# Optimization experiments

Hardware: AMD Instinct MI355X
Metric: run time of the kernel (lower is better)

Reference implementation:

```python
import jax, jax.numpy as jnp
import numpy as np

IN, H1, H2 = 1600, 64, 32

def setup_inputs() -> dict:
    key = jax.random.key(0)
    ks = jax.random.split(key, 8)
    x = jax.random.normal(ks[0], (512, IN), dtype=jnp.float32)
    y = jax.random.normal(ks[1], (512, IN), dtype=jnp.float32)
    # Kaiming-ish init for the MLP params
    W1 = jax.random.normal(ks[2], (IN, H1), dtype=jnp.float32) / np.sqrt(IN)
    b1 = jnp.zeros((H1,), dtype=jnp.float32)
    W2 = jax.random.normal(ks[3], (H1, H2), dtype=jnp.float32) / np.sqrt(H1)
    b2 = jnp.zeros((H2,), dtype=jnp.float32)
    W3 = jax.random.normal(ks[4], (H2, 1), dtype=jnp.float32) / np.sqrt(H2)
    b3 = jnp.zeros((1,), dtype=jnp.float32)
    return {"x": x, "y": y, "W1": W1, "b1": b1, "W2": W2, "b2": b2, "W3": W3, "b3": b3}

def reference(x, y, W1, b1, W2, b2, W3, b3):
    # pairwise difference: (w, qw, 1600)
    d = x[:, None, :] - y[None, :, :]
    h = jax.nn.relu(jnp.einsum('wqi,ih->wqh', d, W1) + b1)   # (w,qw,64)
    h = jax.nn.relu(jnp.einsum('wqh,hk->wqk', h, W2) + b2)   # (w,qw,32)
    o = jax.nn.relu(jnp.einsum('wqk,ko->wqo', h, W3) + b3)   # (w,qw,1)
    return o[..., 0]                                          # (w,qw)
```

## Files before the change

kernel.cpp:

```cpp
#include <hip/hip_runtime.h>
#include <hip/hip_bf16.h>


#define IN_DIM 1600
#define H1D 64
#define H2D 32
#define NROW 512

typedef short bf16x8 __attribute__((ext_vector_type(8)));
typedef float f32x4 __attribute__((ext_vector_type(4)));

static __device__ __forceinline__ short f2bf(float v) {
  __hip_bfloat16 h = __float2bfloat16(v);
  return *reinterpret_cast<short*>(&h);
}

__global__ __launch_bounds__(1024) void proj_kernel(
    const float* __restrict__ x, const float* __restrict__ y,
    const float* __restrict__ W1, const float* __restrict__ b1,
    const float* __restrict__ W2,
    float* __restrict__ P, unsigned short* __restrict__ W2frag) {
  __shared__ float pacc[16 * 4 * 64];
  const int tid = threadIdx.x;
  const int lane = tid & 63;
  const int w = __builtin_amdgcn_readfirstlane(tid >> 6);
  const int row0 = (int)blockIdx.x * 4;
  const float* __restrict__ base = (row0 < NROW) ? x : y;
  const int r0 = (row0 < NROW) ? row0 : row0 - NROW;
  const int k0 = w * (IN_DIM / 16);

  const float* __restrict__ xr0 = base + (size_t)(r0 + 0) * IN_DIM + k0;
  const float* __restrict__ xr1 = base + (size_t)(r0 + 1) * IN_DIM + k0;
  const float* __restrict__ xr2 = base + (size_t)(r0 + 2) * IN_DIM + k0;
  const float* __restrict__ xr3 = base + (size_t)(r0 + 3) * IN_DIM + k0;
  const float* __restrict__ wp = W1 + (size_t)k0 * H1D + lane;

  float a0 = 0.f, a1 = 0.f, a2 = 0.f, a3 = 0.f;
#pragma unroll 4
  for (int i = 0; i < IN_DIM / 16; ++i) {
    const float wv = wp[i * H1D];
    a0 = fmaf(xr0[i], wv, a0);
    a1 = fmaf(xr1[i], wv, a1);
    a2 = fmaf(xr2[i], wv, a2);
    a3 = fmaf(xr3[i], wv, a3);
  }
  pacc[(w * 4 + 0) * 64 + lane] = a0;
  pacc[(w * 4 + 1) * 64 + lane] = a1;
  pacc[(w * 4 + 2) * 64 + lane] = a2;
  pacc[(w * 4 + 3) * 64 + lane] = a3;
  __syncthreads();

  if (tid < 256) {
    const int r = tid >> 6, h = tid & 63;
    float s = 0.f;
#pragma unroll
    for (int ww = 0; ww < 16; ++ww) s += pacc[(ww * 4 + r) * 64 + h];
    if (row0 < NROW) s += b1[h];
    P[(size_t)(row0 + r) * H1D + h] = s;
  } else if (blockIdx.x == 0 && tid >= 512) {
    const int t = tid - 512;
#pragma unroll
    for (int e = t; e < 4 * 64 * 8; e += 512) {
      const int f = e >> 9, l = (e >> 3) & 63, j = e & 7;
      const int ks = f & 1, nt = f >> 1;
      const int k = ks * 32 + (l >> 4) * 8 + j;
      const int n = nt * 16 + (l & 15);
      W2frag[e] = (unsigned short)f2bf(W2[k * H2D + n]);
    }
  }
}

__global__ __launch_bounds__(256) void pair_kernel(
    const float* __restrict__ P, const unsigned short* __restrict__ W2frag,
    const float* __restrict__ b2, const float* __restrict__ W3,
    const float* __restrict__ b3, float* __restrict__ out) {
  __shared__ float sX[16][68];
  __shared__ float sY[16][68];
  __shared__ float sO[16][16];

  const int tid = threadIdx.x;
  const int wave = tid >> 6, lane = tid & 63;
  const int l15 = lane & 15, l4 = lane >> 4;
  const int wb = blockIdx.x * 16, qb = blockIdx.y * 16;

  {
    const int r = tid >> 4, c = (tid & 15) * 4;
    const float4 vx = *reinterpret_cast<const float4*>(&P[(size_t)(wb + r) * H1D + c]);
    const float4 vy = *reinterpret_cast<const float4*>(&P[(size_t)(NROW + qb + r) * H1D + c]);
    *reinterpret_cast<float4*>(&sX[r][c]) = vx;
    *reinterpret_cast<float4*>(&sY[r][c]) = vy;
  }

  bf16x8 bfr[2][2];
#pragma unroll
  for (int nt = 0; nt < 2; ++nt)
#pragma unroll
    for (int ks = 0; ks < 2; ++ks)
      bfr[nt][ks] = *reinterpret_cast<const bf16x8*>(&W2frag[((nt * 2 + ks) * 64 + lane) * 8]);

  f32x4 acc[4][2];
  const float b2v0 = b2[l15], b2v1 = b2[16 + l15];
#pragma unroll
  for (int mt = 0; mt < 4; ++mt)
#pragma unroll
    for (int r = 0; r < 4; ++r) { acc[mt][0][r] = b2v0; acc[mt][1][r] = b2v1; }

  __syncthreads();

#pragma unroll
  for (int ks = 0; ks < 2; ++ks) {
    const int kb = ks * 32 + l4 * 8;
    const float4 y0 = *reinterpret_cast<const float4*>(&sY[l15][kb]);
    const float4 y1 = *reinterpret_cast<const float4*>(&sY[l15][kb + 4]);
#pragma unroll
    for (int mt = 0; mt < 4; ++mt) {
      const int lw = wave * 4 + mt;
      const float4 x0 = *reinterpret_cast<const float4*>(&sX[lw][kb]);
      const float4 x1 = *reinterpret_cast<const float4*>(&sX[lw][kb + 4]);
      bf16x8 af;
      float v;
      v = x0.x - y0.x; af[0] = f2bf(v > 0.f ? v : 0.f);
      v = x0.y - y0.y; af[1] = f2bf(v > 0.f ? v : 0.f);
      v = x0.z - y0.z; af[2] = f2bf(v > 0.f ? v : 0.f);
      v = x0.w - y0.w; af[3] = f2bf(v > 0.f ? v : 0.f);
      v = x1.x - y1.x; af[4] = f2bf(v > 0.f ? v : 0.f);
      v = x1.y - y1.y; af[5] = f2bf(v > 0.f ? v : 0.f);
      v = x1.z - y1.z; af[6] = f2bf(v > 0.f ? v : 0.f);
      v = x1.w - y1.w; af[7] = f2bf(v > 0.f ? v : 0.f);
      acc[mt][0] = __builtin_amdgcn_mfma_f32_16x16x32_bf16(af, bfr[0][ks], acc[mt][0], 0, 0, 0);
      acc[mt][1] = __builtin_amdgcn_mfma_f32_16x16x32_bf16(af, bfr[1][ks], acc[mt][1], 0, 0, 0);
    }
  }

  const float w3v0 = W3[l15], w3v1 = W3[16 + l15];
  const float b3v = b3[0];
#pragma unroll
  for (int mt = 0; mt < 4; ++mt) {
    float t[4];
#pragma unroll
    for (int r = 0; r < 4; ++r) {
      const float q0 = acc[mt][0][r] > 0.f ? acc[mt][0][r] : 0.f;
      const float q1 = acc[mt][1][r] > 0.f ? acc[mt][1][r] : 0.f;
      t[r] = fmaf(q0, w3v0, q1 * w3v1);
    }
#pragma unroll
    for (int off = 1; off < 16; off <<= 1) {
#pragma unroll
      for (int r = 0; r < 4; ++r) t[r] += __shfl_xor(t[r], off, 64);
    }
    if (l15 == 0) {
#pragma unroll
      for (int r = 0; r < 4; ++r) {
        const float o = t[r] + b3v;
        sO[wave * 4 + mt][l4 * 4 + r] = o > 0.f ? o : 0.f;
      }
    }
  }
  __syncthreads();
  out[(size_t)(wb + (tid >> 4)) * NROW + qb + (tid & 15)] = sO[tid >> 4][tid & 15];
}

extern "C" void kernel_launch(void* const* d_in, const int* in_sizes, int n_in,
                              void* d_out, int out_size, void* d_ws, size_t ws_size,
                              hipStream_t stream) {
  const float* x  = (const float*)d_in[0];
  const float* y  = (const float*)d_in[1];
  const float* W1 = (const float*)d_in[2];
  const float* b1 = (const float*)d_in[3];
  const float* W2 = (const float*)d_in[4];
  const float* b2 = (const float*)d_in[5];
  const float* W3 = (const float*)d_in[6];
  const float* b3 = (const float*)d_in[7];
  float* out = (float*)d_out;

  char* ws = (char*)d_ws;
  float* P = (float*)ws;
  unsigned short* W2frag = (unsigned short*)(ws + 1024 * H1D * 4);

  proj_kernel<<<256, 1024, 0, stream>>>(x, y, W1, b1, W2, P, W2frag);
  pair_kernel<<<dim3(32, 32), 256, 0, stream>>>(P, W2frag, b2, W3, b3, out);
}
```

Before: 18.51 us.

## Compute input projection with split-bf16 MFMA and fold W2 conversion into pair kernel

Adds a prep kernel that splits x, y and W1 into bf16 hi/lo parts, written to workspace. The projection becomes an MFMA GEMM using three bf16 products (hi*hi, lo*hi, hi*lo) to keep near-fp32 accuracy. K is split four ways, and the pair kernel sums the partials and adds b1 while staging. W2 is converted to bf16 fragments inside every pair block instead of being precomputed. This trades scalar FMA work for matrix cores, at the cost of an extra launch and about 13 MB of extra global traffic for the bf16 copies.

```diff
diff --git a/kernel.cpp b/kernel.cpp
--- a/kernel.cpp
+++ b/kernel.cpp
@@ -6,74 +6,96 @@
 #define H1D 64
 #define H2D 32
 #define NROW 512
+#define NTOT 1024
+#define KC_TOT 50
+#define KQ 4
 
 typedef short bf16x8 __attribute__((ext_vector_type(8)));
 typedef float f32x4 __attribute__((ext_vector_type(4)));
 
-static __device__ __forceinline__ short f2bf(float v) {
+static __device__ __forceinline__ unsigned short f2bf_u(float v) {
   __hip_bfloat16 h = __float2bfloat16(v);
-  return *reinterpret_cast<short*>(&h);
-}
-
-__global__ __launch_bounds__(1024) void proj_kernel(
+  return *reinterpret_cast<unsigned short*>(&h);
+}
+static __device__ __forceinline__ float bf2f(unsigned short u) {
+  __hip_bfloat16 h = *reinterpret_cast<__hip_bfloat16*>(&u);
+  return __bfloat162float(h);
+}
+
+__global__ __launch_bounds__(256) void prep_kernel(
     const float* __restrict__ x, const float* __restrict__ y,
-    const float* __restrict__ W1, const float* __restrict__ b1,
-    const float* __restrict__ W2,
-    float* __restrict__ P, unsigned short* __restrict__ W2frag) {
-  __shared__ float pacc[16 * 4 * 64];
-  const int tid = threadIdx.x;
-  const int lane = tid & 63;
-  const int w = __builtin_amdgcn_readfirstlane(tid >> 6);
-  const int row0 = (int)blockIdx.x * 4;
-  const float* __restrict__ base = (row0 < NROW) ? x : y;
-  const int r0 = (row0 < NROW) ? row0 : row0 - NROW;
-  const int k0 = w * (IN_DIM / 16);
-
-  const float* __restrict__ xr0 = base + (size_t)(r0 + 0) * IN_DIM + k0;
-  const float* __restrict__ xr1 = base + (size_t)(r0 + 1) * IN_DIM + k0;
-  const float* __restrict__ xr2 = base + (size_t)(r0 + 2) * IN_DIM + k0;
-  const float* __restrict__ xr3 = base + (size_t)(r0 + 3) * IN_DIM + k0;
-  const float* __restrict__ wp = W1 + (size_t)k0 * H1D + lane;
-
-  float a0 = 0.f, a1 = 0.f, a2 = 0.f, a3 = 0.f;
-#pragma unroll 4
-  for (int i = 0; i < IN_DIM / 16; ++i) {
-    const float wv = wp[i * H1D];
-    a0 = fmaf(xr0[i], wv, a0);
-    a1 = fmaf(xr1[i], wv, a1);
-    a2 = fmaf(xr2[i], wv, a2);
-    a3 = fmaf(xr3[i], wv, a3);
-  }
-  pacc[(w * 4 + 0) * 64 + lane] = a0;
-  pacc[(w * 4 + 1) * 64 + lane] = a1;
-  pacc[(w * 4 + 2) * 64 + lane] = a2;
-  pacc[(w * 4 + 3) * 64 + lane] = a3;
-  __syncthreads();
-
-  if (tid < 256) {
-    const int r = tid >> 6, h = tid & 63;
-    float s = 0.f;
-#pragma unroll
-    for (int ww = 0; ww < 16; ++ww) s += pacc[(ww * 4 + r) * 64 + h];
-    if (row0 < NROW) s += b1[h];
-    P[(size_t)(row0 + r) * H1D + h] = s;
-  } else if (blockIdx.x == 0 && tid >= 512) {
-    const int t = tid - 512;
-#pragma unroll
-    for (int e = t; e < 4 * 64 * 8; e += 512) {
-      const int f = e >> 9, l = (e >> 3) & 63, j = e & 7;
-      const int ks = f & 1, nt = f >> 1;
-      const int k = ks * 32 + (l >> 4) * 8 + j;
-      const int n = nt * 16 + (l & 15);
-      W2frag[e] = (unsigned short)f2bf(W2[k * H2D + n]);
-    }
+    const float* __restrict__ W1,
+    unsigned short* __restrict__ XH, unsigned short* __restrict__ XL,
+    unsigned short* __restrict__ WTH, unsigned short* __restrict__ WTL) {
+  const int t = blockIdx.x * 256 + threadIdx.x;
+  if (t < NTOT * 400) {
+    const int row = t / 400;
+    const int k4 = (t % 400) * 4;
+    const float* src = (row < NROW) ? (x + (size_t)row * IN_DIM + k4)
+                                    : (y + (size_t)(row - NROW) * IN_DIM + k4);
+    const float4 v = *reinterpret_cast<const float4*>(src);
+    ushort4 hi, lo;
+    hi.x = f2bf_u(v.x); lo.x = f2bf_u(v.x - bf2f(hi.x));
+    hi.y = f2bf_u(v.y); lo.y = f2bf_u(v.y - bf2f(hi.y));
+    hi.z = f2bf_u(v.z); lo.z = f2bf_u(v.z - bf2f(hi.z));
+    hi.w = f2bf_u(v.w); lo.w = f2bf_u(v.w - bf2f(hi.w));
+    *reinterpret_cast<ushort4*>(&XH[(size_t)row * IN_DIM + k4]) = hi;
+    *reinterpret_cast<ushort4*>(&XL[(size_t)row * IN_DIM + k4]) = lo;
+  } else {
+    const int j = t - NTOT * 400;
+    if (j < H1D * IN_DIM / 2) {
+      const int o = j * 2;
+      const int h = o / IN_DIM, k = o % IN_DIM;
+      const float a = W1[(size_t)k * H1D + h];
+      const float b = W1[(size_t)(k + 1) * H1D + h];
+      ushort2 hh, ll;
+      hh.x = f2bf_u(a); ll.x = f2bf_u(a - bf2f(hh.x));
+      hh.y = f2bf_u(b); ll.y = f2bf_u(b - bf2f(hh.y));
+      *reinterpret_cast<ushort2*>(&WTH[o]) = hh;
+      *reinterpret_cast<ushort2*>(&WTL[o]) = ll;
+    }
+  }
+}
+
+__global__ __launch_bounds__(256) void proj_kernel(
+    const unsigned short* __restrict__ XH, const unsigned short* __restrict__ XL,
+    const unsigned short* __restrict__ WTH, const unsigned short* __restrict__ WTL,
+    float* __restrict__ PTp) {
+  const int tid = threadIdx.x, lane = tid & 63;
+  const int mt = tid >> 6;
+  const int l15 = lane & 15, l4 = lane >> 4;
+  const int nc = (int)blockIdx.x >> 2;
+  const int q = (int)blockIdx.x & 3;
+  const int kc0 = (q * KC_TOT) >> 2, kc1 = ((q + 1) * KC_TOT) >> 2;
+
+  const size_t wrow = (size_t)(mt * 16 + l15) * IN_DIM;
+  const size_t xrow = (size_t)(nc * 16 + l15) * IN_DIM;
+
+  f32x4 aA = {0.f, 0.f, 0.f, 0.f};
+  f32x4 aB = {0.f, 0.f, 0.f, 0.f};
+  f32x4 aC = {0.f, 0.f, 0.f, 0.f};
+  for (int kc = kc0; kc < kc1; ++kc) {
+    const int ko = kc * 32 + l4 * 8;
+    const bf16x8 wh = *reinterpret_cast<const bf16x8*>(&WTH[wrow + ko]);
+    const bf16x8 wl = *reinterpret_cast<const bf16x8*>(&WTL[wrow + ko]);
+    const bf16x8 xh = *reinterpret_cast<const bf16x8*>(&XH[xrow + ko]);
+    const bf16x8 xl = *reinterpret_cast<const bf16x8*>(&XL[xrow + ko]);
+    aA = __builtin_amdgcn_mfma_f32_16x16x32_bf16(wh, xh, aA, 0, 0, 0);
+    aB = __builtin_amdgcn_mfma_f32_16x16x32_bf16(wl, xh, aB, 0, 0, 0);
+    aC = __builtin_amdgcn_mfma_f32_16x16x32_bf16(wh, xl, aC, 0, 0, 0);
+  }
+#pragma unroll
+  for (int r = 0; r < 4; ++r) {
+    const int h = mt * 16 + l4 * 4 + r;
+    PTp[((size_t)q * H1D + h) * NTOT + nc * 16 + l15] = aA[r] + aB[r] + aC[r];
   }
 }
 
 __global__ __launch_bounds__(256) void pair_kernel(
-    const float* __restrict__ P, const unsigned short* __restrict__ W2frag,
-    const float* __restrict__ b2, const float* __restrict__ W3,
-    const float* __restrict__ b3, float* __restrict__ out) {
+    const float* __restrict__ PTp, const float* __restrict__ b1,
+    const float* __restrict__ W2, const float* __restrict__ b2,
+    const float* __restrict__ W3, const float* __restrict__ b3,
+    float* __restrict__ out) {
   __shared__ float sX[16][68];
   __shared__ float sY[16][68];
   __shared__ float sO[16][16];
@@ -84,11 +106,19 @@
   const int wb = blockIdx.x * 16, qb = blockIdx.y * 16;
 
   {
-    const int r = tid >> 4, c = (tid & 15) * 4;
-    const float4 vx = *reinterpret_cast<const float4*>(&P[(size_t)(wb + r) * H1D + c]);
-    const float4 vy = *reinterpret_cast<const float4*>(&P[(size_t)(NROW + qb + r) * H1D + c]);
-    *reinterpret_cast<float4*>(&sX[r][c]) = vx;
-    *reinterpret_cast<float4*>(&sY[r][c]) = vy;
+    const int h = tid >> 2, r0 = (tid & 3) << 2;
+    f32x4 sx = {0.f, 0.f, 0.f, 0.f}, sy = {0.f, 0.f, 0.f, 0.f};
+#pragma unroll
+    for (int q = 0; q < KQ; ++q) {
+      sx += *reinterpret_cast<const f32x4*>(&PTp[((size_t)q * H1D + h) * NTOT + wb + r0]);
+      sy += *reinterpret_cast<const f32x4*>(&PTp[((size_t)q * H1D + h) * NTOT + NROW + qb + r0]);
+    }
+    const float b1h = b1[h];
+#pragma unroll
+    for (int i = 0; i < 4; ++i) {
+      sX[r0 + i][h] = sx[i] + b1h;
+      sY[r0 + i][h] = sy[i];
+    }
   }
 
   bf16x8 bfr[2][2];
@@ -96,10 +126,14 @@
   for (int nt = 0; nt < 2; ++nt)
 #pragma unroll
     for (int ks = 0; ks < 2; ++ks)
-      bfr[nt][ks] = *reinterpret_cast<const bf16x8*>(&W2frag[((nt * 2 + ks) * 64 + lane) * 8]);
+#pragma unroll
+      for (int j = 0; j < 8; ++j)
+        bfr[nt][ks][j] = (short)f2bf_u(W2[(ks * 32 + l4 * 8 + j) * H2D + nt * 16 + l15]);
+  const float b2v0 = b2[l15], b2v1 = b2[16 + l15];
+  const float w3v0 = W3[l15], w3v1 = W3[16 + l15];
+  const float b3v = b3[0];
 
   f32x4 acc[4][2];
-  const float b2v0 = b2[l15], b2v1 = b2[16 + l15];
 #pragma unroll
   for (int mt = 0; mt < 4; ++mt)
 #pragma unroll
@@ -117,23 +151,20 @@
       const int lw = wave * 4 + mt;
       const float4 x0 = *reinterpret_cast<const float4*>(&sX[lw][kb]);
       const float4 x1 = *reinterpret_cast<const float4*>(&sX[lw][kb + 4]);
-      bf16x8 af;
-      float v;
-      v = x0.x - y0.x; af[0] = f2bf(v > 0.f ? v : 0.f);
-      v = x0.y - y0.y; af[1] = f2bf(v > 0.f ? v : 0.f);
-      v = x0.z - y0.z; af[2] = f2bf(v > 0.f ? v : 0.f);
-      v = x0.w - y0.w; af[3] = f2bf(v > 0.f ? v : 0.f);
-      v = x1.x - y1.x; af[4] = f2bf(v > 0.f ? v : 0.f);
-      v = x1.y - y1.y; af[5] = f2bf(v > 0.f ? v : 0.f);
-      v = x1.z - y1.z; af[6] = f2bf(v > 0.f ? v : 0.f);
-      v = x1.w - y1.w; af[7] = f2bf(v > 0.f ? v : 0.f);
+      bf16x8 af; float v;
+      v = x0.x - y0.x; af[0] = (short)f2bf_u(v > 0.f ? v : 0.f);
+      v = x0.y - y0.y; af[1] = (short)f2bf_u(v > 0.f ? v : 0.f);
+      v = x0.z - y0.z; af[2] = (short)f2bf_u(v > 0.f ? v : 0.f);
+      v = x0.w - y0.w; af[3] = (short)f2bf_u(v > 0.f ? v : 0.f);
+      v = x1.x - y1.x; af[4] = (short)f2bf_u(v > 0.f ? v : 0.f);
+      v = x1.y - y1.y; af[5] = (short)f2bf_u(v > 0.f ? v : 0.f);
+      v = x1.z - y1.z; af[6] = (short)f2bf_u(v > 0.f ? v : 0.f);
+      v = x1.w - y1.w; af[7] = (short)f2bf_u(v > 0.f ? v : 0.f);
       acc[mt][0] = __builtin_amdgcn_mfma_f32_16x16x32_bf16(af, bfr[0][ks], acc[mt][0], 0, 0, 0);
       acc[mt][1] = __builtin_amdgcn_mfma_f32_16x16x32_bf16(af, bfr[1][ks], acc[mt][1], 0, 0, 0);
     }
   }
 
-  const float w3v0 = W3[l15], w3v1 = W3[16 + l15];
-  const float b3v = b3[0];
 #pragma unroll
   for (int mt = 0; mt < 4; ++mt) {
     float t[4];
@@ -174,9 +205,13 @@
   float* out = (float*)d_out;
 
   char* ws = (char*)d_ws;
-  float* P = (float*)ws;
-  unsigned short* W2frag = (unsigned short*)(ws + 1024 * H1D * 4);
-
-  proj_kernel<<<256, 1024, 0, stream>>>(x, y, W1, b1, W2, P, W2frag);
-  pair_kernel<<<dim3(32, 32), 256, 0, stream>>>(P, W2frag, b2, W3, b3, out);
-}
+  float* PTp = (float*)ws;
+  unsigned short* XH  = (unsigned short*)(ws + (1u << 20));
+  unsigned short* XL  = (unsigned short*)(ws + (1u << 20) + 3276800u);
+  unsigned short* WTH = (unsigned short*)(ws + (1u << 20) + 2 * 3276800u);
+  unsigned short* WTL = (unsigned short*)(ws + (1u << 20) + 2 * 3276800u + 204800u);
+
+  prep_kernel<<<1800, 256, 0, stream>>>(x, y, W1, XH, XL, WTH, WTL);
+  proj_kernel<<<256, 256, 0, stream>>>(XH, XL, WTH, WTL, PTp);
+  pair_kernel<<<dim3(32, 32), 256, 0, stream>>>(PTp, b1, W2, b2, W3, b3, out);
+}
```

Result: slower. 26.33 us (+42.2%).
